# Kernel optimization log

Measured on AMD Instinct MI355X. Metric: run time of the kernel, lower is better.

The kernel has to match this reference:

```python
import jax, jax.numpy as jnp
import numpy as np

NHLOG2PI = -0.5 * np.log(2.0 * np.pi)


def _log_bessel_i(nu, x):
    # log I_nu(x) via the uniform asymptotic expansion (A&S 9.7.7), accurate for large nu.
    # Replaces the original mpmath besseli loop with a device-friendly closed form.
    z = x / nu
    sq = jnp.sqrt(1.0 + z * z)
    eta = sq + jnp.log(z) - jnp.log1p(sq)
    t = 1.0 / sq
    u1 = (3.0 * t - 5.0 * t ** 3) / 24.0  # first correction term
    return nu * eta - 0.5 * jnp.log(2.0 * jnp.pi * nu) - 0.25 * jnp.log1p(z * z) + jnp.log1p(u1 / nu)


def _log_vmf_partition(d, kappa):
    # log C_d(kappa) = d*(-0.5 log 2pi) + s*log(kappa) - log I_s(kappa), s = d/2 - 1
    s = 0.5 * d - 1.0
    return d * NHLOG2PI + s * jnp.log(kappa) - _log_bessel_i(s, kappa)


def reference(id_samples, kappa_weight, prototypes, targets, project_dim):
    eps_n = 1e-12  # torch F.normalize eps
    eps_c = 1e-8   # torch cosine_similarity eps
    # --- sequential normalized EMA scatter-update of prototypes (faithful to per-sample loop) ---
    norm_samples = id_samples / jnp.maximum(
        jnp.linalg.norm(id_samples, axis=-1, keepdims=True), eps_n)

    def step(protos, inp):
        s_n, t = inp
        new = 0.05 * s_n + 0.95 * protos[t]
        new = new / jnp.maximum(jnp.linalg.norm(new), eps_n)
        return protos.at[t].set(new), None

    protos, _ = jax.lax.scan(step, prototypes, (norm_samples, targets))
    protos = jax.lax.stop_gradient(protos)  # original uses .data.detach()

    # --- cosine similarity [N, C] without materializing the repeated tensors ---
    x_n = id_samples / jnp.maximum(jnp.linalg.norm(id_samples, axis=-1, keepdims=True), eps_c)
    p_n = protos / jnp.maximum(jnp.linalg.norm(protos, axis=-1, keepdims=True), eps_c)
    cos = x_n @ p_n.T  # [N, C]

    kap = jax.nn.relu(kappa_weight)  # [C]
    logits = cos * kap[None, :]
    weight_before_exp = jnp.exp(_log_vmf_partition(float(project_dim), kap))[None, :]  # [1, C]

    # --- weighted vMF NLL ---
    num = weight_before_exp * jnp.exp(logits)
    pred = num / num.sum(-1, keepdims=True)
    p_t = jnp.take_along_axis(pred, targets[:, None], axis=1)[:, 0]
    return -jnp.mean(jnp.log(p_t + 1e-6))


def setup_inputs() -> dict:
    key = jax.random.key(0)
    k1, k2, k3 = jax.random.split(key, 3)
    N, C, D = 16384, 2048, 32
    return {
        "id_samples": jax.random.normal(k1, (N, D), dtype=jnp.float32),
        "kappa_weight": jax.random.uniform(k2, (C,), dtype=jnp.float32),
        "prototypes": jnp.zeros((C, D), dtype=jnp.float32),
        "targets": jax.random.randint(k3, (N,), 0, C),
        "project_dim": D,
    }
```

## Files before the change

### kernel.cpp

```cpp
#include <hip/hip_runtime.h>
#include <hip/hip_bf16.h>
#include <math.h>

#define D 32
#define CAP 28
#define CPB 4
#define SBT 512
#define SSM 16

typedef __attribute__((ext_vector_type(8))) short short8v;
typedef __attribute__((ext_vector_type(4))) float float4v;

static __device__ __forceinline__ unsigned short f2bf(float f) {
    union { __hip_bfloat16 h; unsigned short u; } cv;
    cv.h = __float2bfloat16(f);
    return cv.u;
}

__global__ void __launch_bounds__(64 * CPB)
k_solve(const float* __restrict__ x, const int* __restrict__ tgt,
        const float* __restrict__ p_in, const float* __restrict__ kw,
        unsigned short* __restrict__ qb, float* __restrict__ w,
        int N, int C, float dval) {
    __shared__ int   lcnt[CPB];
    __shared__ int   llist[CPB][CAP];
    __shared__ float R[CPB][29][33];
    __shared__ float G[CPB][28][28];
    __shared__ float gP[CPB][29];
    int tid = threadIdx.x, b = blockIdx.x;
    int lane = tid & 63, wv = tid >> 6;
    int c = b * CPB + wv;
    int e = lane & 31;

    if (tid < CPB) lcnt[tid] = 0;
    __syncthreads();
    for (int i = tid; i < N; i += 64 * CPB) {
        int r = tgt[i] - b * CPB;
        if ((unsigned)r < (unsigned)CPB) {
            int pos = atomicAdd(&lcnt[r], 1);
            if (pos < CAP) llist[r][pos] = i;
        }
    }
    __syncthreads();

    int n = lcnt[wv];
    float kap = fmaxf(kw[c], 0.0f);

    if (n <= CAP) {
        int idx = (lane < n) ? llist[wv][lane] : 0x7fffffff;
        int rank = 0;
        for (int j = 0; j < n; ++j) { int v = __shfl(idx, j); rank += (v < idx) ? 1 : 0; }
        int sorted = idx;
        for (int j = 0; j < n; ++j) {
            int v = __shfl(idx, j); int r = __shfl(rank, j);
            if (r == lane) sorted = v;
        }
        if (lane < D) R[wv][28][e] = p_in[(size_t)c * D + e];
        int half = lane >> 5;
        for (int r0 = 0; r0 < n; r0 += 2) {
            int r = r0 + half;
            int ok = (r < n);
            int si = __shfl(sorted, ok ? r : 0);
            float v = ok ? x[(size_t)si * D + e] : 0.f;
            float ss = v * v;
            ss += __shfl_xor(ss, 16); ss += __shfl_xor(ss, 8); ss += __shfl_xor(ss, 4);
            ss += __shfl_xor(ss, 2);  ss += __shfl_xor(ss, 1);
            if (ok) R[wv][r][e] = v / fmaxf(sqrtf(ss), 1e-12f);
        }

        int T = n * (n - 1) / 2;
        for (int q = lane; q < T; q += 64) {
            int k = (int)((1.0f + sqrtf(1.0f + 8.0f * (float)q)) * 0.5f);
            while (k * (k - 1) / 2 > q) --k;
            while ((k + 1) * k / 2 <= q) ++k;
            int j = q - k * (k - 1) / 2;
            float a0 = 0.f, a1 = 0.f, a2 = 0.f, a3 = 0.f;
            for (int d4 = 0; d4 < D; d4 += 4) {
                a0 = fmaf(R[wv][k][d4],     R[wv][j][d4],     a0);
                a1 = fmaf(R[wv][k][d4 + 1], R[wv][j][d4 + 1], a1);
                a2 = fmaf(R[wv][k][d4 + 2], R[wv][j][d4 + 2], a2);
                a3 = fmaf(R[wv][k][d4 + 3], R[wv][j][d4 + 3], a3);
            }
            G[wv][k][j] = (a0 + a1) + (a2 + a3);
        }
        for (int k = lane; k <= n; k += 64) {
            int kk = (k < n) ? k : 28;
            float a0 = 0.f, a1 = 0.f, a2 = 0.f, a3 = 0.f;
            for (int d4 = 0; d4 < D; d4 += 4) {
                a0 = fmaf(R[wv][kk][d4],     R[wv][28][d4],     a0);
                a1 = fmaf(R[wv][kk][d4 + 1], R[wv][28][d4 + 1], a1);
                a2 = fmaf(R[wv][kk][d4 + 2], R[wv][28][d4 + 2], a2);
                a3 = fmaf(R[wv][kk][d4 + 3], R[wv][28][d4 + 3], a3);
            }
            gP[wv][(k < n) ? k : 28] = (a0 + a1) + (a2 + a3);
        }

        float cc[CAP];
        float cp = 1.0f, U2 = gP[wv][28];
#pragma unroll
        for (int kk = 0; kk < CAP; ++kk) {
            if (kk < n) {
                float dsum = cp * gP[wv][kk];
#pragma unroll
                for (int j = 0; j < CAP; ++j)
                    if (j < kk) dsum = fmaf(cc[j], G[wv][kk][j], dsum);
                float m2 = 0.0025f + fmaf(0.9025f, U2, 0.095f * dsum);
                float m = fmaxf(sqrtf(m2), 1e-12f);
                float binv = 0.95f / m;
                cp *= binv;
#pragma unroll
                for (int j = 0; j < CAP; ++j)
                    if (j < kk) cc[j] *= binv;
                cc[kk] = 0.05f / m;
                U2 = 1.0f;
            }
        }

        float u = cp * R[wv][28][e];
#pragma unroll
        for (int j = 0; j < CAP; ++j)
            if (j < n) u = fmaf(cc[j], R[wv][j][e], u);
        float ss = u * u;
        ss += __shfl_xor(ss, 16); ss += __shfl_xor(ss, 8); ss += __shfl_xor(ss, 4);
        ss += __shfl_xor(ss, 2);  ss += __shfl_xor(ss, 1);
        float pninv = 1.0f / fmaxf(sqrtf(ss), 1e-8f);
        if (lane < D) qb[(size_t)c * D + e] = f2bf(kap * pninv * u);
    } else {
        float p = p_in[(size_t)c * D + e];
        for (int ii = 0; ii < N; ii += 64) {
            unsigned long long mb = __ballot(tgt[ii + lane] == c);
            while (mb) {
                int j = __ffsll(mb) - 1;
                mb &= (mb - 1);
                float v = x[(size_t)(ii + j) * D + e];
                float s2 = v * v;
                s2 += __shfl_xor(s2, 16); s2 += __shfl_xor(s2, 8); s2 += __shfl_xor(s2, 4);
                s2 += __shfl_xor(s2, 2);  s2 += __shfl_xor(s2, 1);
                float s = v / fmaxf(sqrtf(s2), 1e-12f);
                p = fmaf(0.05f, s, 0.95f * p);
                float pp = p * p;
                pp += __shfl_xor(pp, 16); pp += __shfl_xor(pp, 8); pp += __shfl_xor(pp, 4);
                pp += __shfl_xor(pp, 2);  pp += __shfl_xor(pp, 1);
                p = p / fmaxf(sqrtf(pp), 1e-12f);
            }
        }
        float pp = p * p;
        pp += __shfl_xor(pp, 16); pp += __shfl_xor(pp, 8); pp += __shfl_xor(pp, 4);
        pp += __shfl_xor(pp, 2);  pp += __shfl_xor(pp, 1);
        float pn = p / fmaxf(sqrtf(pp), 1e-8f);
        if (lane < D) qb[(size_t)c * D + e] = f2bf(kap * pn);
    }

    if (lane == 0) {
        float nu = 0.5f * dval - 1.0f;
        float z  = kap / nu, z2 = z * z;
        float sq = sqrtf(1.0f + z2);
        float t  = 1.0f / sq;
        float u1 = (3.0f * t - 5.0f * t * t * t) * (1.0f / 24.0f);
        float lw = dval * (-0.918938533204672742f)
                 + nu * (logf(nu) + log1pf(sq) - sq)
                 + 0.5f * logf(6.2831853071795864f * nu)
                 + 0.25f * log1pf(z2)
                 - log1pf(u1 / nu);
        w[c] = __expf(lw);
    }
}

__global__ void __launch_bounds__(SBT)
k_score(const float* __restrict__ x, const int* __restrict__ tgt,
        const unsigned short* __restrict__ qb, const float* __restrict__ w,
        float* __restrict__ part, int N, int C) {
    __shared__ float Sl[8][SSM];
    __shared__ float Lt[SSM];
    int tid = threadIdx.x, b = blockIdx.x;
    int lane = tid & 63, wv = tid >> 6;
    int m = lane & 15, kg = lane >> 4, k0 = kg * 8;
    int s0 = b * SSM;

    short8v a0;
    {
        const float4* px = (const float4*)(x + (size_t)(s0 + m) * D + k0);
        float4 u0 = px[0], u1 = px[1];
        float ss = u0.x*u0.x + u0.y*u0.y + u0.z*u0.z + u0.w*u0.w
                 + u1.x*u1.x + u1.y*u1.y + u1.z*u1.z + u1.w*u1.w;
        ss += __shfl_xor(ss, 16); ss += __shfl_xor(ss, 32);
        float inv = 1.0f / fmaxf(sqrtf(ss), 1e-8f);
        a0[0] = (short)f2bf(u0.x*inv); a0[1] = (short)f2bf(u0.y*inv);
        a0[2] = (short)f2bf(u0.z*inv); a0[3] = (short)f2bf(u0.w*inv);
        a0[4] = (short)f2bf(u1.x*inv); a0[5] = (short)f2bf(u1.y*inv);
        a0[6] = (short)f2bf(u1.z*inv); a0[7] = (short)f2bf(u1.w*inv);
    }

    int tr0[4];
#pragma unroll
    for (int r = 0; r < 4; ++r) tr0[r] = tgt[s0 + kg * 4 + r];

    float4v z = {0.f, 0.f, 0.f, 0.f};
    float4v sa0 = z;
    int ntiles = C >> 7;
    for (int jt = 0; jt < ntiles; ++jt) {
        int c0 = (wv * ntiles + jt) * 16;
        short8v bfrag = *(const short8v*)(qb + (size_t)(c0 + m) * D + k0);
        float wl = w[c0 + m];
        float4v acc0 = __builtin_amdgcn_mfma_f32_16x16x32_bf16(a0, bfrag, z, 0, 0, 0);
#pragma unroll
        for (int r = 0; r < 4; ++r) {
            if (c0 + m == tr0[r]) Lt[kg * 4 + r] = acc0[r];
            sa0[r] = fmaf(wl, __expf(acc0[r]), sa0[r]);
        }
    }
#pragma unroll
    for (int off = 1; off < 16; off <<= 1) {
#pragma unroll
        for (int r = 0; r < 4; ++r) sa0[r] += __shfl_xor(sa0[r], off);
    }
    if (m == 0) {
#pragma unroll
        for (int r = 0; r < 4; ++r) Sl[wv][kg * 4 + r] = sa0[r];
    }
    __syncthreads();

    if (wv == 0) {
        float val = 0.f;
        if (lane < SSM) {
            int s = lane;
            float S = ((Sl[0][s] + Sl[1][s]) + (Sl[2][s] + Sl[3][s]))
                    + ((Sl[4][s] + Sl[5][s]) + (Sl[6][s] + Sl[7][s]));
            int t = tgt[s0 + s];
            val = logf(w[t] * __expf(Lt[s]) / S + 1e-6f);
        }
        val += __shfl_xor(val, 32); val += __shfl_xor(val, 16); val += __shfl_xor(val, 8);
        val += __shfl_xor(val, 4);  val += __shfl_xor(val, 2);  val += __shfl_xor(val, 1);
        if (lane == 0) part[b] = val;
    }
}

__global__ void k_out(const float* __restrict__ part, float* __restrict__ out,
                      int N, int nblk) {
    __shared__ float red[8];
    int tid = threadIdx.x, lane = tid & 63, wv = tid >> 6;
    float v = 0.f;
    if (tid < nblk)       v += part[tid];
    if (tid + 512 < nblk) v += part[tid + 512];
    v += __shfl_xor(v, 32); v += __shfl_xor(v, 16); v += __shfl_xor(v, 8);
    v += __shfl_xor(v, 4);  v += __shfl_xor(v, 2);  v += __shfl_xor(v, 1);
    if (lane == 0) red[wv] = v;
    __syncthreads();
    if (tid == 0)
        out[0] = -(((red[0] + red[1]) + (red[2] + red[3]))
                 + ((red[4] + red[5]) + (red[6] + red[7]))) / (float)N;
}

extern "C" void kernel_launch(void* const* d_in, const int* in_sizes, int n_in,
                              void* d_out, int out_size, void* d_ws, size_t ws_size,
                              hipStream_t stream) {
    const float* x    = (const float*)d_in[0];
    const float* kw   = (const float*)d_in[1];
    const float* p_in = (const float*)d_in[2];
    const int*   tgt  = (const int*)d_in[3];
    int C = in_sizes[1];
    int N = in_sizes[3];
    float dval = (float)(in_sizes[2] / C);
    int nblk = N / SSM;

    unsigned short* qb = (unsigned short*)d_ws;
    float* w    = (float*)(qb + (size_t)C * D);
    float* part = w + C;
    (void)n_in; (void)out_size; (void)ws_size;

    k_solve<<<C / CPB, 64 * CPB, 0, stream>>>(x, tgt, p_in, kw, qb, w, N, C, dval);
    k_score<<<nblk, SBT, 0, stream>>>(x, tgt, qb, w, part, N, C);
    k_out<<<1, 512, 0, stream>>>(part, (float*)d_out, N, nblk);
}
```

Before: 42.81 us.

## Compute per-class sample Gram matrix with bf16 MFMA instead of scalar LDS dot products

The solve kernel now builds each class's Gram matrix of raw samples plus the prototype with four 16x16x32 bf16 MFMA instructions. This replaces the triangular scalar dot-product loops over a normalized LDS copy. Row normalization is folded in afterward through inverse norms taken from the Gram diagonal. The final prototype combination reads the samples straight from global memory rather than from shared memory. In exchange, the Gram entries lose precision because of bf16 inputs, and the final combination adds scattered global loads.

```diff
diff --git a/kernel.cpp b/kernel.cpp
--- a/kernel.cpp
+++ b/kernel.cpp
@@ -16,21 +16,28 @@
     cv.h = __float2bfloat16(f);
     return cv.u;
 }
+static __device__ __forceinline__ short8v cvt8(float4 u0, float4 u1) {
+    short8v o;
+    o[0] = (short)f2bf(u0.x); o[1] = (short)f2bf(u0.y);
+    o[2] = (short)f2bf(u0.z); o[3] = (short)f2bf(u0.w);
+    o[4] = (short)f2bf(u1.x); o[5] = (short)f2bf(u1.y);
+    o[6] = (short)f2bf(u1.z); o[7] = (short)f2bf(u1.w);
+    return o;
+}
 
 __global__ void __launch_bounds__(64 * CPB)
-k_solve(const float* __restrict__ x, const int* __restrict__ tgt,
-        const float* __restrict__ p_in, const float* __restrict__ kw,
-        unsigned short* __restrict__ qb, float* __restrict__ w,
-        int N, int C, float dval) {
+k_gram(const float* __restrict__ x, const int* __restrict__ tgt,
+       const float* __restrict__ p_in, const float* __restrict__ kw,
+       unsigned short* __restrict__ qb, float* __restrict__ w,
+       int N, int C, float dval) {
     __shared__ int   lcnt[CPB];
     __shared__ int   llist[CPB][CAP];
-    __shared__ float R[CPB][29][33];
-    __shared__ float G[CPB][28][28];
-    __shared__ float gP[CPB][29];
+    __shared__ int   slist[CPB][CAP];
+    __shared__ float Graw[CPB][32][33];
+    __shared__ float invv[CPB][32];
     int tid = threadIdx.x, b = blockIdx.x;
     int lane = tid & 63, wv = tid >> 6;
-    int c = b * CPB + wv;
-    int e = lane & 31;
+    int c = b * CPB + wv, e = lane & 31;
 
     if (tid < CPB) lcnt[tid] = 0;
     __syncthreads();
@@ -50,76 +57,67 @@
         int idx = (lane < n) ? llist[wv][lane] : 0x7fffffff;
         int rank = 0;
         for (int j = 0; j < n; ++j) { int v = __shfl(idx, j); rank += (v < idx) ? 1 : 0; }
-        int sorted = idx;
-        for (int j = 0; j < n; ++j) {
-            int v = __shfl(idx, j); int r = __shfl(rank, j);
-            if (r == lane) sorted = v;
-        }
-        if (lane < D) R[wv][28][e] = p_in[(size_t)c * D + e];
-        int half = lane >> 5;
-        for (int r0 = 0; r0 < n; r0 += 2) {
-            int r = r0 + half;
-            int ok = (r < n);
-            int si = __shfl(sorted, ok ? r : 0);
-            float v = ok ? x[(size_t)si * D + e] : 0.f;
-            float ss = v * v;
-            ss += __shfl_xor(ss, 16); ss += __shfl_xor(ss, 8); ss += __shfl_xor(ss, 4);
-            ss += __shfl_xor(ss, 2);  ss += __shfl_xor(ss, 1);
-            if (ok) R[wv][r][e] = v / fmaxf(sqrtf(ss), 1e-12f);
-        }
-
-        int T = n * (n - 1) / 2;
-        for (int q = lane; q < T; q += 64) {
-            int k = (int)((1.0f + sqrtf(1.0f + 8.0f * (float)q)) * 0.5f);
-            while (k * (k - 1) / 2 > q) --k;
-            while ((k + 1) * k / 2 <= q) ++k;
-            int j = q - k * (k - 1) / 2;
-            float a0 = 0.f, a1 = 0.f, a2 = 0.f, a3 = 0.f;
-            for (int d4 = 0; d4 < D; d4 += 4) {
-                a0 = fmaf(R[wv][k][d4],     R[wv][j][d4],     a0);
-                a1 = fmaf(R[wv][k][d4 + 1], R[wv][j][d4 + 1], a1);
-                a2 = fmaf(R[wv][k][d4 + 2], R[wv][j][d4 + 2], a2);
-                a3 = fmaf(R[wv][k][d4 + 3], R[wv][j][d4 + 3], a3);
+        if (lane < n) slist[wv][rank] = idx;
+
+        int m = lane & 15, kg = lane >> 4, k0 = kg * 8;
+        short8v A0 = {0,0,0,0,0,0,0,0}, A1 = {0,0,0,0,0,0,0,0};
+        if (m < n) {
+            const float4* px = (const float4*)(x + (size_t)slist[wv][m] * D + k0);
+            A0 = cvt8(px[0], px[1]);
+        }
+        {
+            int r = 16 + m;
+            if (r < n) {
+                const float4* px = (const float4*)(x + (size_t)slist[wv][r] * D + k0);
+                A1 = cvt8(px[0], px[1]);
+            } else if (r == 31) {
+                const float4* px = (const float4*)(p_in + (size_t)c * D + k0);
+                A1 = cvt8(px[0], px[1]);
             }
-            G[wv][k][j] = (a0 + a1) + (a2 + a3);
-        }
-        for (int k = lane; k <= n; k += 64) {
-            int kk = (k < n) ? k : 28;
-            float a0 = 0.f, a1 = 0.f, a2 = 0.f, a3 = 0.f;
-            for (int d4 = 0; d4 < D; d4 += 4) {
-                a0 = fmaf(R[wv][kk][d4],     R[wv][28][d4],     a0);
-                a1 = fmaf(R[wv][kk][d4 + 1], R[wv][28][d4 + 1], a1);
-                a2 = fmaf(R[wv][kk][d4 + 2], R[wv][28][d4 + 2], a2);
-                a3 = fmaf(R[wv][kk][d4 + 3], R[wv][28][d4 + 3], a3);
-            }
-            gP[wv][(k < n) ? k : 28] = (a0 + a1) + (a2 + a3);
-        }
+        }
+
+        float4v z = {0.f, 0.f, 0.f, 0.f};
+        float4v g00 = __builtin_amdgcn_mfma_f32_16x16x32_bf16(A0, A0, z, 0, 0, 0);
+        float4v g01 = __builtin_amdgcn_mfma_f32_16x16x32_bf16(A0, A1, z, 0, 0, 0);
+        float4v g10 = __builtin_amdgcn_mfma_f32_16x16x32_bf16(A1, A0, z, 0, 0, 0);
+        float4v g11 = __builtin_amdgcn_mfma_f32_16x16x32_bf16(A1, A1, z, 0, 0, 0);
+#pragma unroll
+        for (int r = 0; r < 4; ++r) {
+            int rr = kg * 4 + r;
+            Graw[wv][rr][m]           = g00[r];
+            Graw[wv][rr][16 + m]      = g01[r];
+            Graw[wv][16 + rr][m]      = g10[r];
+            Graw[wv][16 + rr][16 + m] = g11[r];
+        }
+        if (lane < 32)
+            invv[wv][lane] = 1.0f / fmaxf(sqrtf(Graw[wv][lane][lane]), 1e-12f);
 
         float cc[CAP];
-        float cp = 1.0f, U2 = gP[wv][28];
+        float cp = 1.0f, U2 = Graw[wv][31][31];
 #pragma unroll
         for (int kk = 0; kk < CAP; ++kk) {
             if (kk < n) {
-                float dsum = cp * gP[wv][kk];
+                float acc = cp * Graw[wv][kk][31];
 #pragma unroll
                 for (int j = 0; j < CAP; ++j)
-                    if (j < kk) dsum = fmaf(cc[j], G[wv][kk][j], dsum);
+                    if (j < kk) acc = fmaf(cc[j], Graw[wv][kk][j], acc);
+                float dsum = invv[wv][kk] * acc;
                 float m2 = 0.0025f + fmaf(0.9025f, U2, 0.095f * dsum);
-                float m = fmaxf(sqrtf(m2), 1e-12f);
-                float binv = 0.95f / m;
+                float mm = fmaxf(sqrtf(m2), 1e-12f);
+                float binv = 0.95f / mm;
                 cp *= binv;
 #pragma unroll
                 for (int j = 0; j < CAP; ++j)
                     if (j < kk) cc[j] *= binv;
-                cc[kk] = 0.05f / m;
+                cc[kk] = 0.05f * invv[wv][kk] / mm;
                 U2 = 1.0f;
             }
         }
 
-        float u = cp * R[wv][28][e];
+        float u = cp * p_in[(size_t)c * D + e];
 #pragma unroll
         for (int j = 0; j < CAP; ++j)
-            if (j < n) u = fmaf(cc[j], R[wv][j][e], u);
+            if (j < n) u = fmaf(cc[j], x[(size_t)slist[wv][j] * D + e], u);
         float ss = u * u;
         ss += __shfl_xor(ss, 16); ss += __shfl_xor(ss, 8); ss += __shfl_xor(ss, 4);
         ss += __shfl_xor(ss, 2);  ss += __shfl_xor(ss, 1);
@@ -153,7 +151,7 @@
 
     if (lane == 0) {
         float nu = 0.5f * dval - 1.0f;
-        float z  = kap / nu, z2 = z * z;
+        float zz = kap / nu, z2 = zz * zz;
         float sq = sqrtf(1.0f + z2);
         float t  = 1.0f / sq;
         float u1 = (3.0f * t - 5.0f * t * t * t) * (1.0f / 24.0f);
@@ -185,10 +183,10 @@
                  + u1.x*u1.x + u1.y*u1.y + u1.z*u1.z + u1.w*u1.w;
         ss += __shfl_xor(ss, 16); ss += __shfl_xor(ss, 32);
         float inv = 1.0f / fmaxf(sqrtf(ss), 1e-8f);
-        a0[0] = (short)f2bf(u0.x*inv); a0[1] = (short)f2bf(u0.y*inv);
-        a0[2] = (short)f2bf(u0.z*inv); a0[3] = (short)f2bf(u0.w*inv);
-        a0[4] = (short)f2bf(u1.x*inv); a0[5] = (short)f2bf(u1.y*inv);
-        a0[6] = (short)f2bf(u1.z*inv); a0[7] = (short)f2bf(u1.w*inv);
+        float4 v0, v1;
+        v0.x = u0.x*inv; v0.y = u0.y*inv; v0.z = u0.z*inv; v0.w = u0.w*inv;
+        v1.x = u1.x*inv; v1.y = u1.y*inv; v1.z = u1.z*inv; v1.w = u1.w*inv;
+        a0 = cvt8(v0, v1);
     }
 
     int tr0[4];
@@ -268,7 +266,7 @@
     float* part = w + C;
     (void)n_in; (void)out_size; (void)ws_size;
 
-    k_solve<<<C / CPB, 64 * CPB, 0, stream>>>(x, tgt, p_in, kw, qb, w, N, C, dval);
+    k_gram<<<C / CPB, 64 * CPB, 0, stream>>>(x, tgt, p_in, kw, qb, w, N, C, dval);
     k_score<<<nblk, SBT, 0, stream>>>(x, tgt, qb, w, part, N, C);
     k_out<<<1, 512, 0, stream>>>(part, (float*)d_out, N, nblk);
 }
```

New measurement: 39.16 us. -8.5%, faster.
